# Kernel tuning notes

Measured on AMD Instinct MI355X. Metric: run time of the kernel, lower is better.

Reference implementation:

```python
import jax, jax.numpy as jnp
import numpy as np

I, H, O = 64, 512, 64
B, S = 32, 2048


def setup_inputs() -> dict:
    key = jax.random.key(0)
    ks = jax.random.split(key, 8)
    def xavier(k, shape):
        fan_in, fan_out = shape[1], shape[0]
        lim = jnp.sqrt(6.0 / (fan_in + fan_out))
        return jax.random.uniform(k, shape, jnp.float32, -lim, lim)
    return {
        "x": jax.random.normal(ks[0], (B, S, I), jnp.float32),
        "h_0": jnp.zeros((B, H), jnp.float32),
        "Wz": xavier(ks[1], (H, I + H)),
        "Wr": xavier(ks[2], (H, I + H)),
        "Wh": xavier(ks[3], (H, I + H)),
        "bz": jnp.ones((H,), jnp.float32),
        "br": jnp.zeros((H,), jnp.float32),
        "bh": jnp.zeros((H,), jnp.float32),
        "W1": xavier(ks[4], (H, H)),
        "b1": jnp.zeros((H,), jnp.float32),
        "W2": xavier(ks[5], (O, H)),
        "b2": jnp.zeros((O,), jnp.float32),
    }


def reference(x, h_0, Wz, Wr, Wh, bz, br, bh, W1, b1, W2, b2):
    def step(h_prev, x_t):
        combined = jnp.concatenate([x_t, h_prev], axis=1)          # [B, I+H]
        z = jax.nn.sigmoid(combined @ Wz.T + bz)                   # [B, H]
        r = jax.nn.sigmoid(combined @ Wr.T + br)                   # [B, H]
        gate_input = jnp.concatenate([r * h_prev, x_t], axis=1)    # [B, H+I]
        h_hat = jnp.tanh(gate_input @ Wh.T + bh)                   # [B, H]
        h_t = (1.0 - z) * h_prev + z * h_hat
        out = jax.nn.relu(h_t @ W1.T + b1) @ W2.T + b2             # [B, O]
        return h_t, out

    # scan over time: x -> [S, B, I]
    h_last, outs = jax.lax.scan(step, h_0, jnp.swapaxes(x, 0, 1))
    return jnp.swapaxes(outs, 0, 1), h_last  # [B, S, O], [B, H]
```

## Files before the change

kernel.cpp:

```cpp
#include <hip/hip_runtime.h>
#include <stdint.h>

#define S_LEN 2048

typedef unsigned long long u64;
typedef unsigned int u32;
typedef __attribute__((ext_vector_type(8))) short short8;
typedef __attribute__((ext_vector_type(4))) float f32x4;

#define XIDX(pbuf, grp, m, c) (((((pbuf)*2 + (grp))*16 + (m))*512) + (c))

__device__ __forceinline__ unsigned short f2bf(float f) {
  union { float f; u32 u; } v; v.f = f;
  u32 u = v.u;
  u = (u + 0x7FFFu + ((u >> 16) & 1u)) >> 16;
  return (unsigned short)u;
}
__device__ __forceinline__ float bf2f(u32 lo16) {
  union { u32 u; float f; } v; v.u = lo16 << 16; return v.f;
}
__device__ __forceinline__ u32 cvt2bf(float lo, float hi) {
  u32 r; asm("v_cvt_pk_bf16_f32 %0, %1, %2" : "=v"(r) : "v"(lo), "v"(hi)); return r;
}
__device__ __forceinline__ void st_u32(u32* p, u32 v) {
  __hip_atomic_store(p, v, __ATOMIC_RELAXED, __HIP_MEMORY_SCOPE_AGENT);
}
__device__ __forceinline__ u32 ld_u32(const u32* p) {
  return __hip_atomic_load(p, __ATOMIC_RELAXED, __HIP_MEMORY_SCOPE_AGENT);
}
__device__ __forceinline__ u64 ld_u64a(const u64* p) {
  return __hip_atomic_load(p, __ATOMIC_RELAXED, __HIP_MEMORY_SCOPE_AGENT);
}
__device__ __forceinline__ u32 detag(u64 q) {
  return (u32)(q & 0xFFFFu) | (u32)((q >> 16) & 0xFFFF0000u);
}

__device__ __forceinline__ void probe16(const u32* Xgrp, u32 tag, int lane) {
  const u32* p = Xgrp + (lane & 15) * 32;
  unsigned it = 0;
  for (;;) {
    u32 v = ld_u32(p);
    if (__all((int)((v >> 16) == tag))) break;
    if (++it > (1u << 22)) break;
  }
}

__device__ __forceinline__ void stage_quarter(const u32* Xgrp, u64 pat, int kq, int lane,
                                              unsigned short* Adst) {
  const u64* base = (const u64*)(Xgrp + (lane & 15) * 512 + kq * 128 + ((lane >> 4) << 3));
  u64 r[16];
  for (unsigned it = 0;; ++it) {
    u64 acc = 0;
#pragma unroll
    for (int c = 0; c < 4; ++c)
#pragma unroll
      for (int q = 0; q < 4; ++q) {
        u64 v = ld_u64a(base + c * 16 + q);
        r[c * 4 + q] = v;
        acc |= v ^ pat;
      }
    if (__all((int)((acc & 0xFFFF0000FFFF0000ULL) == 0))) break;
    if (it > (1u << 20)) break;
  }
#pragma unroll
  for (int c = 0; c < 4; ++c) {
    uint4 pk;
    pk.x = detag(r[c * 4 + 0]); pk.y = detag(r[c * 4 + 1]);
    pk.z = detag(r[c * 4 + 2]); pk.w = detag(r[c * 4 + 3]);
    *(uint4*)(Adst + (size_t)((kq * 4 + c) * 64 + lane) * 8) = pk;
  }
}

__device__ __forceinline__ f32x4 gemm_lds(const unsigned short* Bb, const unsigned short* A,
                                          int lane, short8 xa0, short8 xa1) {
  f32x4 a0 = {0.f, 0.f, 0.f, 0.f}, a1 = {0.f, 0.f, 0.f, 0.f};
  a0 = __builtin_amdgcn_mfma_f32_16x16x32_bf16(xa0, *(const short8*)(Bb + 0 * 512), a0, 0, 0, 0);
  a1 = __builtin_amdgcn_mfma_f32_16x16x32_bf16(xa1, *(const short8*)(Bb + 1 * 512), a1, 0, 0, 0);
#pragma unroll
  for (int kk = 0; kk < 16; kk += 2) {
    short8 u = *(const short8*)(A + (size_t)(kk * 64 + lane) * 8);
    short8 v = *(const short8*)(A + (size_t)((kk + 1) * 64 + lane) * 8);
    a0 = __builtin_amdgcn_mfma_f32_16x16x32_bf16(u, *(const short8*)(Bb + (kk + 2) * 512), a0, 0, 0, 0);
    a1 = __builtin_amdgcn_mfma_f32_16x16x32_bf16(v, *(const short8*)(Bb + (kk + 3) * 512), a1, 0, 0, 0);
  }
  return a0 + a1;
}

__global__ void prep_kernel(const float* __restrict__ Wz, const float* __restrict__ Wr,
                            const float* __restrict__ Wh, const float* __restrict__ W1,
                            const float* __restrict__ W2,
                            unsigned short* __restrict__ WgT,
                            unsigned short* __restrict__ W1T,
                            unsigned short* __restrict__ W2T) {
  const int total = 1536 * 576 + 512 * 512 + 64 * 512;
  for (int idx = blockIdx.x * 256 + threadIdx.x; idx < total; idx += gridDim.x * 256) {
    if (idx < 1536 * 576) {
      int row = idx / 576, k = idx % 576;
      float v;
      if (row < 512)       v = Wz[row * 576 + k];
      else if (row < 1024) v = Wr[(row - 512) * 576 + k];
      else {
        int r = row - 1024;
        v = (k < 64) ? Wh[r * 576 + 512 + k] : Wh[r * 576 + (k - 64)];
      }
      WgT[idx] = f2bf(v);
    } else if (idx < 1536 * 576 + 512 * 512) {
      int i = idx - 1536 * 576;
      W1T[i] = f2bf(W1[i]);
    } else {
      int i = idx - 1536 * 576 - 512 * 512;
      W2T[i] = f2bf(W2[i]);
    }
  }
}

__global__ void __launch_bounds__(256, 1) recur_kernel(
    const float* __restrict__ x, const float* __restrict__ h0,
    const float* __restrict__ bz, const float* __restrict__ br,
    const float* __restrict__ bh, const unsigned short* __restrict__ WgT,
    u32* __restrict__ Hx, u32* __restrict__ RHx,
    unsigned short* __restrict__ h_all, float* __restrict__ h_last) {
  extern __shared__ char smem[];
  unsigned short* Wf  = (unsigned short*)smem;
  unsigned short* Ah  = Wf + 6 * 18 * 64 * 8;
  unsigned short* Arh = Ah + 16 * 64 * 8;

  const int wg = blockIdx.x;
  const int g = wg >> 4, w = wg & 15;
  const int tid = threadIdx.x;
  const int lane = tid & 63, wave = tid >> 6;
  const int crow = (lane >> 4) << 2;
  const int ccol = lane & 15;
  const int ko8 = (lane >> 4) << 3;

  for (int i = tid; i < 6 * 18 * 64; i += 256) {
    int T = i / (18 * 64);
    int kk = (i >> 6) % 18;
    int l = i & 63;
    int row = (T >> 1) * 512 + w * 32 + (T & 1) * 16 + (l & 15);
    int k = kk * 32 + ((l >> 4) << 3);
    uint4 v = *(const uint4*)(WgT + (size_t)row * 576 + k);
    *(uint4*)(Wf + (size_t)i * 8) = v;
  }
  for (int i = tid; i < 512; i += 256) {
    int m = i >> 5, c = i & 31;
    float hv = h0[(size_t)(g * 16 + m) * 512 + w * 32 + c];
    st_u32(Hx + XIDX(0, g, m, w * 32 + c), (u32)f2bf(hv));
  }
  __syncthreads();

  const float* xrow = x + (size_t)(g * 16 + ccol) * (S_LEN * 64) + ko8;
  const bool is_zh = (wave < 2);
  const int nloc = (wave & 1) * 16 + ccol;
  const int colg = w * 32 + nloc;
  const float bzv = is_zh ? bz[colg] : 0.f;
  const float bhv = is_zh ? bh[colg] : 0.f;
  const float brv = is_zh ? 0.f : br[colg];
  const unsigned short* Bza = Wf + (size_t)wave * 18 * 512 + lane * 8;
  const unsigned short* Bh  = Wf + (size_t)(4 + (wave & 1)) * 18 * 512 + lane * 8;

  float hold[4];
  if (is_zh) {
#pragma unroll
    for (int j = 0; j < 4; ++j)
      hold[j] = h0[(size_t)(g * 16 + crow + j) * 512 + colg];
  }

  float4 p0 = *(const float4*)(xrow);
  float4 p1 = *(const float4*)(xrow + 4);
  float4 p2 = *(const float4*)(xrow + 32);
  float4 p3 = *(const float4*)(xrow + 36);

  for (int t = 0; t < S_LEN; ++t) {
    const int pb = t & 1;
    const u32 tag = (u32)t;
    const u64 pat = ((u64)tag << 16) | ((u64)tag << 48);
    u32* Hgrp  = Hx  + XIDX(pb, g, 0, 0);
    u32* RHgrp = RHx + XIDX(pb, g, 0, 0);

    short8 xa0, xa1;
    {
      union { u32 w4[4]; short8 v; } u;
      u.w4[0] = cvt2bf(p0.x, p0.y); u.w4[1] = cvt2bf(p0.z, p0.w);
      u.w4[2] = cvt2bf(p1.x, p1.y); u.w4[3] = cvt2bf(p1.z, p1.w);
      xa0 = u.v;
      u.w4[0] = cvt2bf(p2.x, p2.y); u.w4[1] = cvt2bf(p2.z, p2.w);
      u.w4[2] = cvt2bf(p3.x, p3.y); u.w4[3] = cvt2bf(p3.z, p3.w);
      xa1 = u.v;
    }

    probe16(Hgrp, tag, lane);
    stage_quarter(Hgrp, pat, wave, lane, Ah);
    __syncthreads();

    float zv[4];
    if (is_zh) {
      f32x4 zacc = gemm_lds(Bza, Ah, lane, xa0, xa1);
#pragma unroll
      for (int j = 0; j < 4; ++j)
        zv[j] = 1.f / (1.f + __expf(-(zacc[j] + bzv)));
    } else {
      f32x4 racc = gemm_lds(Bza, Ah, lane, xa0, xa1);
#pragma unroll
      for (int j = 0; j < 4; ++j) {
        u32 hbf = Ah[(size_t)((w * 4 + (nloc >> 3)) * 16 + 0) * 0 +
                     (size_t)((w) * 64 + ((nloc >> 3) << 4) + (crow + j)) * 8 + (nloc & 7)];
        float rv = 1.f / (1.f + __expf(-(racc[j] + brv)));
        float rh = rv * bf2f(hbf);
        st_u32(RHx + XIDX(pb, g, crow + j, colg), (tag << 16) | (u32)f2bf(rh));
      }
    }

    {
      const float* xn = xrow + (size_t)((t + 1 < S_LEN) ? t + 1 : t) * 64;
      p0 = *(const float4*)(xn);      p1 = *(const float4*)(xn + 4);
      p2 = *(const float4*)(xn + 32); p3 = *(const float4*)(xn + 36);
    }

    probe16(RHgrp, tag, lane);
    stage_quarter(RHgrp, pat, wave, lane, Arh);
    __syncthreads();

    if (is_zh) {
      f32x4 hacc = gemm_lds(Bh, Arh, lane, xa0, xa1);
#pragma unroll
      for (int j = 0; j < 4; ++j) {
        float e = __expf(2.f * (hacc[j] + bhv));
        float hh = 1.f - 2.f / (e + 1.f);
        float hn = (1.f - zv[j]) * hold[j] + zv[j] * hh;
        hold[j] = hn;
        unsigned short hbv = f2bf(hn);
        st_u32(Hx + XIDX(pb ^ 1, g, crow + j, colg), ((u32)(t + 1) << 16) | hbv);
        h_all[((size_t)(g * 16 + crow + j) * S_LEN + t) * 512 + colg] = hbv;
        if (t == S_LEN - 1) h_last[(size_t)(g * 16 + crow + j) * 512 + colg] = hn;
      }
    }
  }
}

__global__ void __launch_bounds__(256, 1) head_kernel(
    const unsigned short* __restrict__ h_all, const unsigned short* __restrict__ W1T,
    const unsigned short* __restrict__ W2T, const float* __restrict__ b1,
    const float* __restrict__ b2, float* __restrict__ out) {
  extern __shared__ char smem[];
  unsigned short* hs = (unsigned short*)smem;
  unsigned short* act = hs + 64 * 520;

  const int tid = threadIdx.x, lane = tid & 63, wave = tid >> 6;
  const int crow = (lane >> 4) << 2, ccol = lane & 15;
  const size_t row0 = (size_t)blockIdx.x * 64;

  for (int i = tid; i < 64 * 64; i += 256) {
    int r = i >> 6, c8 = i & 63;
    uint4 v = *(const uint4*)(h_all + (row0 + r) * 512 + c8 * 8);
    *(uint4*)(hs + r * 520 + c8 * 8) = v;
  }
  __syncthreads();

  f32x4 acc[8][4];
#pragma unroll
  for (int nt = 0; nt < 8; ++nt)
#pragma unroll
    for (int mt = 0; mt < 4; ++mt) acc[nt][mt] = {0.f, 0.f, 0.f, 0.f};

  for (int k = 0; k < 16; ++k) {
    short8 a[4];
#pragma unroll
    for (int mt = 0; mt < 4; ++mt)
      a[mt] = *(const short8*)(hs + (mt * 16 + ccol) * 520 + k * 32 + ((lane >> 4) << 3));
#pragma unroll
    for (int nt = 0; nt < 8; ++nt) {
      int n0 = (wave * 8 + nt) * 16;
      short8 b = *(const short8*)(W1T + (size_t)(n0 + ccol) * 512 + k * 32 + ((lane >> 4) << 3));
#pragma unroll
      for (int mt = 0; mt < 4; ++mt)
        acc[nt][mt] = __builtin_amdgcn_mfma_f32_16x16x32_bf16(a[mt], b, acc[nt][mt], 0, 0, 0);
    }
  }
#pragma unroll
  for (int nt = 0; nt < 8; ++nt) {
    int n = wave * 128 + nt * 16 + ccol;
    float bias = b1[n];
#pragma unroll
    for (int mt = 0; mt < 4; ++mt)
#pragma unroll
      for (int j = 0; j < 4; ++j) {
        float v = fmaxf(acc[nt][mt][j] + bias, 0.f);
        act[(mt * 16 + crow + j) * 520 + n] = f2bf(v);
      }
  }
  __syncthreads();
  for (int i = tid; i < 64 * 64; i += 256) {
    int r = i >> 6, c8 = i & 63;
    uint4 v = *(const uint4*)(W2T + (size_t)r * 512 + c8 * 8);
    *(uint4*)(hs + r * 520 + c8 * 8) = v;
  }
  __syncthreads();

  f32x4 acc2[4];
#pragma unroll
  for (int nt = 0; nt < 4; ++nt) acc2[nt] = {0.f, 0.f, 0.f, 0.f};
  for (int k = 0; k < 16; ++k) {
    short8 a = *(const short8*)(act + (wave * 16 + ccol) * 520 + k * 32 + ((lane >> 4) << 3));
#pragma unroll
    for (int nt = 0; nt < 4; ++nt) {
      short8 b = *(const short8*)(hs + (nt * 16 + ccol) * 520 + k * 32 + ((lane >> 4) << 3));
      acc2[nt] = __builtin_amdgcn_mfma_f32_16x16x32_bf16(a, b, acc2[nt], 0, 0, 0);
    }
  }
#pragma unroll
  for (int nt = 0; nt < 4; ++nt) {
    int o = nt * 16 + ccol;
    float bias = b2[o];
#pragma unroll
    for (int j = 0; j < 4; ++j) {
      int r = wave * 16 + crow + j;
      out[(row0 + r) * 64 + o] = acc2[nt][j] + bias;
    }
  }
}

extern "C" void kernel_launch(void* const* d_in, const int* in_sizes, int n_in,
                              void* d_out, int out_size, void* d_ws, size_t ws_size,
                              hipStream_t stream) {
  const float* x  = (const float*)d_in[0];
  const float* h0 = (const float*)d_in[1];
  const float* Wz = (const float*)d_in[2];
  const float* Wr = (const float*)d_in[3];
  const float* Wh = (const float*)d_in[4];
  const float* bz = (const float*)d_in[5];
  const float* br = (const float*)d_in[6];
  const float* bh = (const float*)d_in[7];
  const float* W1 = (const float*)d_in[8];
  const float* b1 = (const float*)d_in[9];
  const float* W2 = (const float*)d_in[10];
  const float* b2 = (const float*)d_in[11];

  char* ws = (char*)d_ws;
  size_t off = 0;
  u32* Hx  = (u32*)(ws + off); off += (size_t)2 * 2 * 16 * 512 * 4;
  u32* RHx = (u32*)(ws + off); off += (size_t)2 * 2 * 16 * 512 * 4;
  unsigned short* WgT   = (unsigned short*)(ws + off); off += (size_t)1536 * 576 * 2;
  unsigned short* W1T   = (unsigned short*)(ws + off); off += (size_t)512 * 512 * 2;
  unsigned short* W2T   = (unsigned short*)(ws + off); off += (size_t)64 * 512 * 2;
  unsigned short* h_all = (unsigned short*)(ws + off); off += (size_t)32 * 2048 * 512 * 2;

  float* out = (float*)d_out;
  float* h_last = out + (size_t)32 * 2048 * 64;

  hipLaunchKernelGGL(prep_kernel, dim3(1024), dim3(256), 0, stream,
                     Wz, Wr, Wh, W1, W2, WgT, W1T, W2T);

  const int recur_lds = (6 * 18 * 64 * 8 + 2 * 16 * 64 * 8) * 2;
  hipFuncSetAttribute(reinterpret_cast<const void*>(&recur_kernel),
                      hipFuncAttributeMaxDynamicSharedMemorySize, recur_lds);
  hipLaunchKernelGGL(recur_kernel, dim3(32), dim3(256), recur_lds, stream,
                     x, h0, bz, br, bh, WgT, Hx, RHx, h_all, h_last);

  const int head_lds = 2 * 64 * 520 * 2;
  hipFuncSetAttribute(reinterpret_cast<const void*>(&head_kernel),
                      hipFuncAttributeMaxDynamicSharedMemorySize, head_lds);
  hipLaunchKernelGGL(head_kernel, dim3(1024), dim3(256), head_lds, stream,
                     h_all, W1T, W2T, b1, b2, out);
}
```

Before: 16.99 ms.

## Split recurrence into Z/R and H wave pairs with LDS-flag sync

Each workgroup's recurrence is split into two wave pairs. Waves 2-3 compute both the z and r gates and publish r*h and z through global tagged buffers (a new Zx buffer). Waves 0-1 compute the candidate state and the state update. The block-wide __syncthreads is replaced by pairwise LDS flag spinning, and relaxed stores become atomic exchanges. Polling now uses a single-word spin between full reloads. The aim is to let the two gate stages of neighbouring timesteps overlap and to cut barrier cost, at the price of an extra global round trip for z and more register pressure from 32-entry staging arrays.

After: 26.93 ms. +58.5%, slower.

```diff
diff --git a/kernel.cpp b/kernel.cpp
--- a/kernel.cpp
+++ b/kernel.cpp
@@ -2,6 +2,7 @@
 #include <stdint.h>
 
 #define S_LEN 2048
+#define TAGM64 0xFFFF0000FFFF0000ULL
 
 typedef unsigned long long u64;
 typedef unsigned int u32;
@@ -22,8 +23,8 @@
 __device__ __forceinline__ u32 cvt2bf(float lo, float hi) {
   u32 r; asm("v_cvt_pk_bf16_f32 %0, %1, %2" : "=v"(r) : "v"(lo), "v"(hi)); return r;
 }
-__device__ __forceinline__ void st_u32(u32* p, u32 v) {
-  __hip_atomic_store(p, v, __ATOMIC_RELAXED, __HIP_MEMORY_SCOPE_AGENT);
+__device__ __forceinline__ void ax_swap(u32* p, u32 v) {
+  (void)__hip_atomic_exchange(p, v, __ATOMIC_RELAXED, __HIP_MEMORY_SCOPE_AGENT);
 }
 __device__ __forceinline__ u32 ld_u32(const u32* p) {
   return __hip_atomic_load(p, __ATOMIC_RELAXED, __HIP_MEMORY_SCOPE_AGENT);
@@ -34,56 +35,13 @@
 __device__ __forceinline__ u32 detag(u64 q) {
   return (u32)(q & 0xFFFFu) | (u32)((q >> 16) & 0xFFFF0000u);
 }
-
-__device__ __forceinline__ void probe16(const u32* Xgrp, u32 tag, int lane) {
-  const u32* p = Xgrp + (lane & 15) * 32;
-  unsigned it = 0;
-  for (;;) {
-    u32 v = ld_u32(p);
-    if (__all((int)((v >> 16) == tag))) break;
-    if (++it > (1u << 22)) break;
-  }
-}
-
-__device__ __forceinline__ void stage_quarter(const u32* Xgrp, u64 pat, int kq, int lane,
-                                              unsigned short* Adst) {
-  const u64* base = (const u64*)(Xgrp + (lane & 15) * 512 + kq * 128 + ((lane >> 4) << 3));
-  u64 r[16];
-  for (unsigned it = 0;; ++it) {
-    u64 acc = 0;
-#pragma unroll
-    for (int c = 0; c < 4; ++c)
-#pragma unroll
-      for (int q = 0; q < 4; ++q) {
-        u64 v = ld_u64a(base + c * 16 + q);
-        r[c * 4 + q] = v;
-        acc |= v ^ pat;
-      }
-    if (__all((int)((acc & 0xFFFF0000FFFF0000ULL) == 0))) break;
-    if (it > (1u << 20)) break;
-  }
-#pragma unroll
-  for (int c = 0; c < 4; ++c) {
-    uint4 pk;
-    pk.x = detag(r[c * 4 + 0]); pk.y = detag(r[c * 4 + 1]);
-    pk.z = detag(r[c * 4 + 2]); pk.w = detag(r[c * 4 + 3]);
-    *(uint4*)(Adst + (size_t)((kq * 4 + c) * 64 + lane) * 8) = pk;
-  }
-}
-
-__device__ __forceinline__ f32x4 gemm_lds(const unsigned short* Bb, const unsigned short* A,
-                                          int lane, short8 xa0, short8 xa1) {
-  f32x4 a0 = {0.f, 0.f, 0.f, 0.f}, a1 = {0.f, 0.f, 0.f, 0.f};
-  a0 = __builtin_amdgcn_mfma_f32_16x16x32_bf16(xa0, *(const short8*)(Bb + 0 * 512), a0, 0, 0, 0);
-  a1 = __builtin_amdgcn_mfma_f32_16x16x32_bf16(xa1, *(const short8*)(Bb + 1 * 512), a1, 0, 0, 0);
-#pragma unroll
-  for (int kk = 0; kk < 16; kk += 2) {
-    short8 u = *(const short8*)(A + (size_t)(kk * 64 + lane) * 8);
-    short8 v = *(const short8*)(A + (size_t)((kk + 1) * 64 + lane) * 8);
-    a0 = __builtin_amdgcn_mfma_f32_16x16x32_bf16(u, *(const short8*)(Bb + (kk + 2) * 512), a0, 0, 0, 0);
-    a1 = __builtin_amdgcn_mfma_f32_16x16x32_bf16(v, *(const short8*)(Bb + (kk + 3) * 512), a1, 0, 0, 0);
-  }
-  return a0 + a1;
+__device__ __forceinline__ void lds_fence() {
+  asm volatile("s_waitcnt lgkmcnt(0)" ::: "memory");
+}
+
+__device__ __forceinline__ short8 mfma_bf16(short8 a, short8 b, f32x4& acc) {
+  acc = __builtin_amdgcn_mfma_f32_16x16x32_bf16(a, b, acc, 0, 0, 0);
+  return a;
 }
 
 __global__ void prep_kernel(const float* __restrict__ Wz, const float* __restrict__ Wr,
@@ -118,12 +76,13 @@
     const float* __restrict__ x, const float* __restrict__ h0,
     const float* __restrict__ bz, const float* __restrict__ br,
     const float* __restrict__ bh, const unsigned short* __restrict__ WgT,
-    u32* __restrict__ Hx, u32* __restrict__ RHx,
+    u32* __restrict__ Hx, u32* __restrict__ RHx, u32* __restrict__ Zx,
     unsigned short* __restrict__ h_all, float* __restrict__ h_last) {
   extern __shared__ char smem[];
   unsigned short* Wf  = (unsigned short*)smem;
   unsigned short* Ah  = Wf + 6 * 18 * 64 * 8;
   unsigned short* Arh = Ah + 16 * 64 * 8;
+  volatile u32* slots = (volatile u32*)(Arh + 16 * 64 * 8);
 
   const int wg = blockIdx.x;
   const int g = wg >> 4, w = wg & 15;
@@ -145,94 +104,185 @@
   for (int i = tid; i < 512; i += 256) {
     int m = i >> 5, c = i & 31;
     float hv = h0[(size_t)(g * 16 + m) * 512 + w * 32 + c];
-    st_u32(Hx + XIDX(0, g, m, w * 32 + c), (u32)f2bf(hv));
-  }
+    ax_swap(Hx + XIDX(0, g, m, w * 32 + c), (u32)f2bf(hv));
+  }
+  if (tid < 4) slots[tid] = 0;
   __syncthreads();
 
   const float* xrow = x + (size_t)(g * 16 + ccol) * (S_LEN * 64) + ko8;
-  const bool is_zh = (wave < 2);
-  const int nloc = (wave & 1) * 16 + ccol;
-  const int colg = w * 32 + nloc;
-  const float bzv = is_zh ? bz[colg] : 0.f;
-  const float bhv = is_zh ? bh[colg] : 0.f;
-  const float brv = is_zh ? 0.f : br[colg];
-  const unsigned short* Bza = Wf + (size_t)wave * 18 * 512 + lane * 8;
-  const unsigned short* Bh  = Wf + (size_t)(4 + (wave & 1)) * 18 * 512 + lane * 8;
-
-  float hold[4];
-  if (is_zh) {
+
+  if (wave >= 2) {
+    const int half = wave - 2;
+    const int anloc = half * 16 + ccol;
+    const int colA = w * 32 + anloc;
+    const float brv = br[colA], bzv = bz[colA];
+    const unsigned short* BZ = Wf + (size_t)half * 18 * 512 + lane * 8;
+    const unsigned short* BR = Wf + (size_t)(2 + half) * 18 * 512 + lane * 8;
+
+    for (int t = 0; t < S_LEN; ++t) {
+      const int pb = t & 1;
+      const u32 tag = (u32)t;
+      const u64 pat = ((u64)tag << 16) | ((u64)tag << 48);
+      const u32* Hgrp = Hx + XIDX(pb, g, 0, 0);
+
+      short8 xa0, xa1;
+      {
+        const float* xp = xrow + (size_t)t * 64;
+        float4 q0 = *(const float4*)(xp), q1 = *(const float4*)(xp + 4);
+        float4 q2 = *(const float4*)(xp + 32), q3 = *(const float4*)(xp + 36);
+        union { u32 w4[4]; short8 v; } u;
+        u.w4[0] = cvt2bf(q0.x, q0.y); u.w4[1] = cvt2bf(q0.z, q0.w);
+        u.w4[2] = cvt2bf(q1.x, q1.y); u.w4[3] = cvt2bf(q1.z, q1.w);
+        xa0 = u.v;
+        u.w4[0] = cvt2bf(q2.x, q2.y); u.w4[1] = cvt2bf(q2.z, q2.w);
+        u.w4[2] = cvt2bf(q3.x, q3.y); u.w4[3] = cvt2bf(q3.z, q3.w);
+        xa1 = u.v;
+      }
+
+      u64 r[32];
+      const u64* base = (const u64*)(Hgrp + ccol * 512 + half * 256 + ko8);
+      for (unsigned it = 0;; ++it) {
+        u64 acc = 0;
+#pragma unroll
+        for (int c = 0; c < 8; ++c)
+#pragma unroll
+          for (int q = 0; q < 4; ++q) {
+            u64 v = ld_u64a(base + c * 16 + q);
+            r[c * 4 + q] = v;
+            acc |= v ^ pat;
+          }
+        if (__all((int)((acc & TAGM64) == 0ULL))) break;
+        if (it > (1u << 20)) break;
+        unsigned it2 = 0;
+        u64 s;
+        do { s = ld_u64a(base); } while ((((s ^ pat) & TAGM64) != 0ULL) && ++it2 < (1u << 22));
+      }
+#pragma unroll
+      for (int c = 0; c < 8; ++c) {
+        uint4 pk;
+        pk.x = detag(r[c * 4 + 0]); pk.y = detag(r[c * 4 + 1]);
+        pk.z = detag(r[c * 4 + 2]); pk.w = detag(r[c * 4 + 3]);
+        *(uint4*)(Ah + (size_t)((half * 8 + c) * 64 + lane) * 8) = pk;
+      }
+      lds_fence();
+      if (lane == 0) slots[2 + half] = t + 1;
+      { unsigned it = 0; while (slots[2 + (half ^ 1)] < (u32)(t + 1) && ++it < (1u << 22)) {} }
+      lds_fence();
+
+      f32x4 aZ = {0.f, 0.f, 0.f, 0.f}, aR = {0.f, 0.f, 0.f, 0.f};
+      mfma_bf16(xa0, *(const short8*)(BZ + 0), aZ);
+      mfma_bf16(xa0, *(const short8*)(BR + 0), aR);
+      mfma_bf16(xa1, *(const short8*)(BZ + 512), aZ);
+      mfma_bf16(xa1, *(const short8*)(BR + 512), aR);
+#pragma unroll
+      for (int kk = 0; kk < 16; ++kk) {
+        short8 af = *(const short8*)(Ah + (size_t)(kk * 64 + lane) * 8);
+        mfma_bf16(af, *(const short8*)(BZ + (size_t)(kk + 2) * 512), aZ);
+        mfma_bf16(af, *(const short8*)(BR + (size_t)(kk + 2) * 512), aR);
+      }
+
+      float rv[4];
+#pragma unroll
+      for (int j = 0; j < 4; ++j) {
+        rv[j] = 1.f / (1.f + __expf(-(aR[j] + brv)));
+        u32 hw = *(volatile unsigned short*)(Ah +
+                 (size_t)(w * 64 + ((anloc >> 3) << 4) + crow + j) * 8 + (anloc & 7));
+        float rh = rv[j] * bf2f(hw);
+        ax_swap(RHx + XIDX(pb, g, crow + j, colA), (tag << 16) | (u32)f2bf(rh));
+      }
+#pragma unroll
+      for (int j = 0; j < 4; ++j) {
+        float zv = 1.f / (1.f + __expf(-(aZ[j] + bzv)));
+        ax_swap(Zx + XIDX(pb, g, crow + j, colA), (tag << 16) | (u32)f2bf(zv));
+      }
+    }
+  } else {
+    const int nloc = wave * 16 + ccol;
+    const int colB = w * 32 + nloc;
+    const float bhv = bh[colB];
+    const unsigned short* BH = Wf + (size_t)(4 + wave) * 18 * 512 + lane * 8;
+    float hold[4];
 #pragma unroll
     for (int j = 0; j < 4; ++j)
-      hold[j] = h0[(size_t)(g * 16 + crow + j) * 512 + colg];
-  }
-
-  float4 p0 = *(const float4*)(xrow);
-  float4 p1 = *(const float4*)(xrow + 4);
-  float4 p2 = *(const float4*)(xrow + 32);
-  float4 p3 = *(const float4*)(xrow + 36);
-
-  for (int t = 0; t < S_LEN; ++t) {
-    const int pb = t & 1;
-    const u32 tag = (u32)t;
-    const u64 pat = ((u64)tag << 16) | ((u64)tag << 48);
-    u32* Hgrp  = Hx  + XIDX(pb, g, 0, 0);
-    u32* RHgrp = RHx + XIDX(pb, g, 0, 0);
-
-    short8 xa0, xa1;
-    {
-      union { u32 w4[4]; short8 v; } u;
-      u.w4[0] = cvt2bf(p0.x, p0.y); u.w4[1] = cvt2bf(p0.z, p0.w);
-      u.w4[2] = cvt2bf(p1.x, p1.y); u.w4[3] = cvt2bf(p1.z, p1.w);
-      xa0 = u.v;
-      u.w4[0] = cvt2bf(p2.x, p2.y); u.w4[1] = cvt2bf(p2.z, p2.w);
-      u.w4[2] = cvt2bf(p3.x, p3.y); u.w4[3] = cvt2bf(p3.z, p3.w);
-      xa1 = u.v;
-    }
-
-    probe16(Hgrp, tag, lane);
-    stage_quarter(Hgrp, pat, wave, lane, Ah);
-    __syncthreads();
-
-    float zv[4];
-    if (is_zh) {
-      f32x4 zacc = gemm_lds(Bza, Ah, lane, xa0, xa1);
-#pragma unroll
-      for (int j = 0; j < 4; ++j)
-        zv[j] = 1.f / (1.f + __expf(-(zacc[j] + bzv)));
-    } else {
-      f32x4 racc = gemm_lds(Bza, Ah, lane, xa0, xa1);
+      hold[j] = h0[(size_t)(g * 16 + crow + j) * 512 + colB];
+
+    for (int t = 0; t < S_LEN; ++t) {
+      const int pb = t & 1;
+      const u32 tag = (u32)t;
+      const u64 pat = ((u64)tag << 16) | ((u64)tag << 48);
+      const u32* RHgrp = RHx + XIDX(pb, g, 0, 0);
+
+      short8 xa0, xa1;
+      {
+        const float* xp = xrow + (size_t)t * 64;
+        float4 q0 = *(const float4*)(xp), q1 = *(const float4*)(xp + 4);
+        float4 q2 = *(const float4*)(xp + 32), q3 = *(const float4*)(xp + 36);
+        union { u32 w4[4]; short8 v; } u;
+        u.w4[0] = cvt2bf(q0.x, q0.y); u.w4[1] = cvt2bf(q0.z, q0.w);
+        u.w4[2] = cvt2bf(q1.x, q1.y); u.w4[3] = cvt2bf(q1.z, q1.w);
+        xa0 = u.v;
+        u.w4[0] = cvt2bf(q2.x, q2.y); u.w4[1] = cvt2bf(q2.z, q2.w);
+        u.w4[2] = cvt2bf(q3.x, q3.y); u.w4[3] = cvt2bf(q3.z, q3.w);
+        xa1 = u.v;
+      }
+
+      u64 r[32];
+      u32 zr[4];
+      const u64* base = (const u64*)(RHgrp + ccol * 512 + wave * 256 + ko8);
+      const u32* zp = Zx + XIDX(pb, g, crow, colB);
+      for (unsigned it = 0;; ++it) {
+        u64 acc = 0;
+#pragma unroll
+        for (int c = 0; c < 8; ++c)
+#pragma unroll
+          for (int q = 0; q < 4; ++q) {
+            u64 v = ld_u64a(base + c * 16 + q);
+            r[c * 4 + q] = v;
+            acc |= v ^ pat;
+          }
+#pragma unroll
+        for (int j = 0; j < 4; ++j) {
+          zr[j] = ld_u32(zp + j * 512);
+          acc |= (u64)((zr[j] ^ (tag << 16)) & 0xFFFF0000u);
+        }
+        if (__all((int)((acc & TAGM64) == 0ULL))) break;
+        if (it > (1u << 20)) break;
+        unsigned it2 = 0;
+        u64 s;
+        do { s = ld_u64a(base); } while ((((s ^ pat) & TAGM64) != 0ULL) && ++it2 < (1u << 22));
+      }
+#pragma unroll
+      for (int c = 0; c < 8; ++c) {
+        uint4 pk;
+        pk.x = detag(r[c * 4 + 0]); pk.y = detag(r[c * 4 + 1]);
+        pk.z = detag(r[c * 4 + 2]); pk.w = detag(r[c * 4 + 3]);
+        *(uint4*)(Arh + (size_t)((wave * 8 + c) * 64 + lane) * 8) = pk;
+      }
+      lds_fence();
+      if (lane == 0) slots[wave] = t + 1;
+      { unsigned it = 0; while (slots[wave ^ 1] < (u32)(t + 1) && ++it < (1u << 22)) {} }
+      lds_fence();
+
+      f32x4 hc = {0.f, 0.f, 0.f, 0.f};
+      mfma_bf16(xa0, *(const short8*)(BH + 0), hc);
+      mfma_bf16(xa1, *(const short8*)(BH + 512), hc);
+#pragma unroll
+      for (int kk = 0; kk < 16; ++kk) {
+        short8 af = *(const short8*)(Arh + (size_t)(kk * 64 + lane) * 8);
+        mfma_bf16(af, *(const short8*)(BH + (size_t)(kk + 2) * 512), hc);
+      }
+
 #pragma unroll
       for (int j = 0; j < 4; ++j) {
-        u32 hbf = Ah[(size_t)((w * 4 + (nloc >> 3)) * 16 + 0) * 0 +
-                     (size_t)((w) * 64 + ((nloc >> 3) << 4) + (crow + j)) * 8 + (nloc & 7)];
-        float rv = 1.f / (1.f + __expf(-(racc[j] + brv)));
-        float rh = rv * bf2f(hbf);
-        st_u32(RHx + XIDX(pb, g, crow + j, colg), (tag << 16) | (u32)f2bf(rh));
-      }
-    }
-
-    {
-      const float* xn = xrow + (size_t)((t + 1 < S_LEN) ? t + 1 : t) * 64;
-      p0 = *(const float4*)(xn);      p1 = *(const float4*)(xn + 4);
-      p2 = *(const float4*)(xn + 32); p3 = *(const float4*)(xn + 36);
-    }
-
-    probe16(RHgrp, tag, lane);
-    stage_quarter(RHgrp, pat, wave, lane, Arh);
-    __syncthreads();
-
-    if (is_zh) {
-      f32x4 hacc = gemm_lds(Bh, Arh, lane, xa0, xa1);
-#pragma unroll
-      for (int j = 0; j < 4; ++j) {
-        float e = __expf(2.f * (hacc[j] + bhv));
+        float e = __expf(2.f * (hc[j] + bhv));
         float hh = 1.f - 2.f / (e + 1.f);
-        float hn = (1.f - zv[j]) * hold[j] + zv[j] * hh;
+        float zf = bf2f(zr[j] & 0xFFFFu);
+        float hn = (1.f - zf) * hold[j] + zf * hh;
         hold[j] = hn;
         unsigned short hbv = f2bf(hn);
-        st_u32(Hx + XIDX(pb ^ 1, g, crow + j, colg), ((u32)(t + 1) << 16) | hbv);
-        h_all[((size_t)(g * 16 + crow + j) * S_LEN + t) * 512 + colg] = hbv;
-        if (t == S_LEN - 1) h_last[(size_t)(g * 16 + crow + j) * 512 + colg] = hn;
+        ax_swap(Hx + XIDX(pb ^ 1, g, crow + j, colB), ((tag + 1) << 16) | hbv);
+        h_all[((size_t)(g * 16 + crow + j) * S_LEN + t) * 512 + colB] = hbv;
+        if (t == S_LEN - 1) h_last[(size_t)(g * 16 + crow + j) * 512 + colB] = hn;
       }
     }
   }
@@ -340,6 +390,7 @@
   size_t off = 0;
   u32* Hx  = (u32*)(ws + off); off += (size_t)2 * 2 * 16 * 512 * 4;
   u32* RHx = (u32*)(ws + off); off += (size_t)2 * 2 * 16 * 512 * 4;
+  u32* Zx  = (u32*)(ws + off); off += (size_t)2 * 2 * 16 * 512 * 4;
   unsigned short* WgT   = (unsigned short*)(ws + off); off += (size_t)1536 * 576 * 2;
   unsigned short* W1T   = (unsigned short*)(ws + off); off += (size_t)512 * 512 * 2;
   unsigned short* W2T   = (unsigned short*)(ws + off); off += (size_t)64 * 512 * 2;
@@ -351,11 +402,11 @@
   hipLaunchKernelGGL(prep_kernel, dim3(1024), dim3(256), 0, stream,
                      Wz, Wr, Wh, W1, W2, WgT, W1T, W2T);
 
-  const int recur_lds = (6 * 18 * 64 * 8 + 2 * 16 * 64 * 8) * 2;
+  const int recur_lds = (6 * 18 * 64 * 8 + 2 * 16 * 64 * 8) * 2 + 32;
   hipFuncSetAttribute(reinterpret_cast<const void*>(&recur_kernel),
                       hipFuncAttributeMaxDynamicSharedMemorySize, recur_lds);
   hipLaunchKernelGGL(recur_kernel, dim3(32), dim3(256), recur_lds, stream,
-                     x, h0, bz, br, bh, WgT, Hx, RHx, h_all, h_last);
+                     x, h0, bz, br, bh, WgT, Hx, RHx, Zx, h_all, h_last);
 
   const int head_lds = 2 * 64 * 520 * 2;
   hipFuncSetAttribute(reinterpret_cast<const void*>(&head_kernel),
```
